# Kernel optimization log

Hardware: AMD Instinct MI355X
Metric: run time of the kernel (lower is better)

The kernel has to match this reference:

```python
import jax, jax.numpy as jnp
import numpy as np

BETA = 1.0
DECAY = 0.95


def setup_inputs() -> dict:
    key = jax.random.key(0)
    ks = jax.random.split(key, 10)
    B, S, D = 8, 2048, 1024
    M, d = 4096, 256
    sc_in = 1.0 / np.sqrt(D)
    sc_slot = 1.0 / np.sqrt(d)
    return {
        "x": jax.random.normal(ks[0], (B, S, D), jnp.float32),
        "memory": jax.random.normal(ks[1], (B, M, d), jnp.float32) * 0.01,
        "Wq": jax.random.normal(ks[2], (D, d), jnp.float32) * sc_in,
        "bq": jnp.zeros((d,), jnp.float32),
        "Wv": jax.random.normal(ks[3], (D, d), jnp.float32) * sc_in,
        "bv": jnp.zeros((d,), jnp.float32),
        "Wo": jax.random.normal(ks[4], (d, D), jnp.float32) * sc_slot,
        "bo": jnp.zeros((D,), jnp.float32),
        "Wg": jax.random.normal(ks[5], (D, 1), jnp.float32) * sc_in,
        "bg": jnp.zeros((1,), jnp.float32),
    }


def reference(x, memory, Wq, bq, Wv, bv, Wo, bo, Wg, bg):
    # ---- shared summary + query ----
    x_summary = jnp.mean(x, axis=1)                      # [B, D]
    query = x_summary @ Wq + bq                          # [B, d]

    # ---- read: Hopfield retrieval against memory[0] (shared patterns) ----
    patterns = memory[0]                                 # [M, d]
    read_scores = BETA * (query @ patterns.T)            # [B, M]
    read_attn = jax.nn.softmax(read_scores, axis=-1)
    retrieved = read_attn @ patterns                     # [B, d]
    read_out = retrieved @ Wo + bo                       # [B, D]
    x_augmented = x + read_out[:, None, :]               # broadcast over seq

    # ---- write: gated EMA update to per-batch memory ----
    write_value = x_summary @ Wv + bv                    # [B, d]
    write_gate = jax.nn.sigmoid(x_summary @ Wg + bg)     # [B, 1]
    w_scores = BETA * jnp.einsum('bd,bmd->bm', query, memory)
    w_attn = jax.nn.softmax(w_scores, axis=-1)           # [B, M]
    update = write_gate[:, :, None] * write_value[:, None, :]   # [B, 1, d]
    weighted_update = w_attn[:, :, None] * update        # [B, M, d]
    memory_new = DECAY * memory + (1.0 - DECAY) * weighted_update

    return x_augmented, memory_new
```

## Files before the change

### kernel.cpp

```cpp
#include <hip/hip_runtime.h>
#include <math.h>

#define BB 8
#define SS 2048
#define DD 1024
#define MM 4096
#define dd 256
#define NCH 64
#define CS (SS/NCH)

#define OFF_PART  0
#define OFF_Q     524288
#define OFF_WV    526336
#define OFF_GATE  528384
#define OFF_COMBO 528392
#define OFF_SUMS  528400
#define OFF_SC    528416
#define OFF_PRET  593952
#define OFF_ROUT  725024

__global__ void k1(const float* __restrict__ x, float* __restrict__ ws) {
    int blk = blockIdx.x;
    int chunk = blk & 63;
    int b = blk >> 6;
    int t = threadIdx.x;
    const float4* x4 = (const float4*)(x + ((size_t)b*SS + (size_t)chunk*CS)*DD);
    float4 a = make_float4(0.f,0.f,0.f,0.f);
    #pragma unroll 8
    for (int s = 0; s < CS; ++s) {
        float4 v = x4[s*(DD/4) + t];
        a.x += v.x; a.y += v.y; a.z += v.z; a.w += v.w;
    }
    ((float4*)(ws + OFF_PART))[(size_t)(b*NCH + chunk)*256 + t] = a;
}

__global__ void k23(const float* __restrict__ Wq, const float* __restrict__ bq,
                    const float* __restrict__ Wv, const float* __restrict__ bv,
                    const float* __restrict__ Wg, const float* __restrict__ bg,
                    float* __restrict__ ws) {
    __shared__ float4 xsA[256];
    __shared__ float4 xsB[256];
    __shared__ float red[512];
    int blk = blockIdx.x;
    int t = threadIdx.x;
    if (blk < 64) {
        int cs = blk & 3;
        int wb = blk >> 2;
        int b = wb & 7;
        int which = wb >> 3;
        int col4 = t & 255;
        int half = t >> 8;
        const float4* p4 = (const float4*)(ws + OFF_PART);
        float4 a = make_float4(0.f,0.f,0.f,0.f);
        #pragma unroll 8
        for (int c = 0; c < 32; ++c) {
            float4 v = p4[(size_t)(b*NCH + half*32 + c)*256 + col4];
            a.x += v.x; a.y += v.y; a.z += v.z; a.w += v.w;
        }
        if (half == 0) xsA[col4] = a; else xsB[col4] = a;
        __syncthreads();
        if (t < 256) {
            float4 u = xsA[t], v = xsB[t];
            xsA[t] = make_float4((u.x+v.x)*(1.f/SS), (u.y+v.y)*(1.f/SS),
                                 (u.z+v.z)*(1.f/SS), (u.w+v.w)*(1.f/SS));
        }
        __syncthreads();
        const float* xs = (const float*)xsA;
        const float* W = which ? Wv : Wq;
        int kg = t >> 6;
        int c0 = cs*64 + (t & 63);
        float acc = 0.f;
        #pragma unroll 8
        for (int kk = 0; kk < 128; ++kk) {
            int k = kg*128 + kk;
            acc += xs[k] * W[(size_t)k*dd + c0];
        }
        red[t] = acc;
        __syncthreads();
        if (t < 64) {
            int c = cs*64 + t;
            float o = red[t] + red[t+64] + red[t+128] + red[t+192]
                    + red[t+256] + red[t+320] + red[t+384] + red[t+448];
            o += which ? bv[c] : bq[c];
            ws[(which ? OFF_WV : OFF_Q) + b*dd + c] = o;
        }
    } else {
        int b = blk - 64;
        const float* base = ws + OFF_PART + (size_t)(b*NCH)*DD;
        float wg0 = Wg[t], wg1 = Wg[t + 512];
        float acc = 0.f;
        #pragma unroll 8
        for (int c = 0; c < NCH; ++c) {
            const float* p = base + (size_t)c*DD;
            acc += p[t]*wg0 + p[t+512]*wg1;
        }
        red[t] = acc; __syncthreads();
        for (int s2 = 256; s2 > 0; s2 >>= 1) {
            if (t < s2) red[t] += red[t + s2];
            __syncthreads();
        }
        if (t == 0)
            ws[OFF_GATE + b] = 1.f / (1.f + __expf(-(red[0]*(1.f/SS) + bg[0])));
    }
}

__global__ void k4(const float* __restrict__ memory, float* __restrict__ ws) {
    int wave = threadIdx.x >> 6;
    int lane = threadIdx.x & 63;
    int task = blockIdx.x*4 + wave;
    int m = task & (MM-1);
    int b = (task >> 12) & 7;
    int which = task >> 15;
    const float* row = (which == 0) ? (memory + (size_t)m*dd)
                                    : (memory + ((size_t)b*MM + m)*dd);
    const float4 a  = ((const float4*)row)[lane];
    const float4 qv = ((const float4*)(ws + OFF_Q + b*dd))[lane];
    float p = a.x*qv.x + a.y*qv.y + a.z*qv.z + a.w*qv.w;
    #pragma unroll
    for (int off = 32; off > 0; off >>= 1) p += __shfl_xor(p, off);
    if (lane == 0) ws[OFF_SC + (size_t)(which*BB + b)*MM + m] = __expf(p);
}

__global__ void k5(const float* __restrict__ memory, float* __restrict__ ws) {
    __shared__ float red[256];
    int blk = blockIdx.x;
    int t = threadIdx.x;
    if (blk < 16) {
        const float4* p = (const float4*)(ws + OFF_SC + (size_t)blk*MM);
        float s = 0.f;
        #pragma unroll
        for (int i = 0; i < 4; ++i) {
            float4 v = p[i*256 + t];
            s += v.x + v.y + v.z + v.w;
        }
        red[t] = s; __syncthreads();
        for (int s2 = 128; s2 > 0; s2 >>= 1) {
            if (t < s2) red[t] += red[t + s2];
            __syncthreads();
        }
        if (t == 0) ws[OFF_SUMS + blk] = red[0];
    } else {
        int idx = blk - 16;
        int mc = idx & 63;
        int b = idx >> 6;
        if (t < 64) red[t] = ws[OFF_SC + (size_t)b*MM + mc*64 + t];
        __syncthreads();
        float acc = 0.f;
        const float* pat = memory + (size_t)mc*64*dd + t;
        #pragma unroll 8
        for (int i = 0; i < 64; ++i) acc += red[i] * pat[(size_t)i*dd];
        ws[OFF_PRET + (size_t)(b*64 + mc)*dd + t] = acc;
    }
}

__global__ void k7(const float* __restrict__ Wo, const float* __restrict__ bo,
                   float* __restrict__ ws) {
    __shared__ float ret[dd];
    __shared__ float red[256];
    int blk = blockIdx.x;
    int cb = blk & 15;
    int b = blk >> 4;
    int t = threadIdx.x;
    float acc0 = 0.f;
    #pragma unroll 8
    for (int mc = 0; mc < 64; ++mc)
        acc0 += ws[OFF_PRET + (size_t)(b*64 + mc)*dd + t];
    ret[t] = acc0 / ws[OFF_SUMS + b];
    if (cb == 0 && t == 0)
        ws[OFF_COMBO + b] = 0.05f * ws[OFF_GATE + b] / ws[OFF_SUMS + BB + b];
    __syncthreads();
    int c = t & 63, jr = t >> 6;
    float acc = 0.f;
    #pragma unroll 8
    for (int jj = 0; jj < 64; ++jj) {
        int j = jr*64 + jj;
        acc += ret[j] * Wo[(size_t)j*DD + cb*64 + c];
    }
    red[t] = acc; __syncthreads();
    if (t < 64) {
        ws[OFF_ROUT + (size_t)b*DD + cb*64 + t] =
            red[t] + red[t+64] + red[t+128] + red[t+192] + bo[cb*64 + t];
    }
}

__global__ void k8(const float* __restrict__ x, const float* __restrict__ memory,
                   const float* __restrict__ ws, float* __restrict__ out) {
    const int NA = BB*SS*DD/4;
    const int NT = NA + BB*MM*dd/4;
    const float4* x4 = (const float4*)x;
    const float4* m4 = (const float4*)memory;
    const float4* r4 = (const float4*)(ws + OFF_ROUT);
    const float4* w4 = (const float4*)(ws + OFF_WV);
    float4* o4 = (float4*)out;
    int stride = gridDim.x * blockDim.x;
    for (int i = blockIdx.x*blockDim.x + threadIdx.x; i < NT; i += stride) {
        if (i < NA) {
            int b = i >> 19;
            int c = i & 255;
            float4 xv = x4[i];
            float4 rv = r4[(b << 8) + c];
            o4[i] = make_float4(xv.x+rv.x, xv.y+rv.y, xv.z+rv.z, xv.w+rv.w);
        } else {
            int j = i - NA;
            int b = j >> 18;
            int m = (j >> 6) & (MM-1);
            int d4 = j & 63;
            float coeff = ws[OFF_COMBO + b] * ws[OFF_SC + (size_t)(BB + b)*MM + m];
            float4 wv = w4[(b << 6) + d4];
            float4 mv = m4[j];
            o4[i] = make_float4(0.95f*mv.x + coeff*wv.x,
                                0.95f*mv.y + coeff*wv.y,
                                0.95f*mv.z + coeff*wv.z,
                                0.95f*mv.w + coeff*wv.w);
        }
    }
}

extern "C" void kernel_launch(void* const* d_in, const int* in_sizes, int n_in,
                              void* d_out, int out_size, void* d_ws, size_t ws_size,
                              hipStream_t stream) {
    const float* x      = (const float*)d_in[0];
    const float* memory = (const float*)d_in[1];
    const float* Wq     = (const float*)d_in[2];
    const float* bq     = (const float*)d_in[3];
    const float* Wv     = (const float*)d_in[4];
    const float* bv     = (const float*)d_in[5];
    const float* Wo     = (const float*)d_in[6];
    const float* bo     = (const float*)d_in[7];
    const float* Wg     = (const float*)d_in[8];
    const float* bg     = (const float*)d_in[9];
    float* out = (float*)d_out;
    float* ws  = (float*)d_ws;

    k1<<<BB*NCH, 256, 0, stream>>>(x, ws);
    k23<<<72, 512, 0, stream>>>(Wq, bq, Wv, bv, Wg, bg, ws);
    k4<<<2*BB*MM/4, 256, 0, stream>>>(memory, ws);
    k5<<<16 + BB*64, 256, 0, stream>>>(memory, ws);
    k7<<<BB*16, 256, 0, stream>>>(Wo, bo, ws);
    k8<<<4096, 256, 0, stream>>>(x, memory, ws, out);
}
```

Before: 76.76 us.

## Fuse score, partial-sum and retrieval kernels into one tiled kernel

Merges the per-row score kernel and the sum/retrieval kernel into a single kernel. Each block handles a 64-row memory tile: it computes exp scores into shared memory, writes a per-tile partial sum, and either does the pattern-weighted retrieval (read path) or stores the scores (write path). The final sums are then reduced inside k7, so one launch goes away and the exp scores no longer make a round trip through global memory for the retrieval step. The cost is a longer per-block serial loop over 64 rows and a little extra reduction work in k7.

```diff
diff --git a/kernel.cpp b/kernel.cpp
--- a/kernel.cpp
+++ b/kernel.cpp
@@ -14,10 +14,10 @@
 #define OFF_WV    526336
 #define OFF_GATE  528384
 #define OFF_COMBO 528392
-#define OFF_SUMS  528400
-#define OFF_SC    528416
-#define OFF_PRET  593952
-#define OFF_ROUT  725024
+#define OFF_SUMP  528400
+#define OFF_SC    529424
+#define OFF_PRET  562192
+#define OFF_ROUT  693264
 
 __global__ void k1(const float* __restrict__ x, float* __restrict__ ws) {
     int blk = blockIdx.x;
@@ -43,6 +43,7 @@
     __shared__ float red[512];
     int blk = blockIdx.x;
     int t = threadIdx.x;
+    const float4* p4 = (const float4*)(ws + OFF_PART);
     if (blk < 64) {
         int cs = blk & 3;
         int wb = blk >> 2;
@@ -50,7 +51,6 @@
         int which = wb >> 3;
         int col4 = t & 255;
         int half = t >> 8;
-        const float4* p4 = (const float4*)(ws + OFF_PART);
         float4 a = make_float4(0.f,0.f,0.f,0.f);
         #pragma unroll 8
         for (int c = 0; c < 32; ++c) {
@@ -104,52 +104,40 @@
     }
 }
 
-__global__ void k4(const float* __restrict__ memory, float* __restrict__ ws) {
-    int wave = threadIdx.x >> 6;
-    int lane = threadIdx.x & 63;
-    int task = blockIdx.x*4 + wave;
-    int m = task & (MM-1);
-    int b = (task >> 12) & 7;
-    int which = task >> 15;
-    const float* row = (which == 0) ? (memory + (size_t)m*dd)
-                                    : (memory + ((size_t)b*MM + m)*dd);
-    const float4 a  = ((const float4*)row)[lane];
+__global__ void k45(const float* __restrict__ memory, float* __restrict__ ws) {
+    __shared__ float esc[64];
+    int idx = blockIdx.x;
+    int which = idx >> 9;
+    int b = (idx >> 6) & 7;
+    int mc = idx & 63;
+    int t = threadIdx.x;
+    int wave = t >> 6, lane = t & 63;
+    const float* tile = ((which == 0) ? memory : memory + (size_t)b*MM*dd)
+                        + (size_t)mc*64*dd;
     const float4 qv = ((const float4*)(ws + OFF_Q + b*dd))[lane];
-    float p = a.x*qv.x + a.y*qv.y + a.z*qv.z + a.w*qv.w;
-    #pragma unroll
-    for (int off = 32; off > 0; off >>= 1) p += __shfl_xor(p, off);
-    if (lane == 0) ws[OFF_SC + (size_t)(which*BB + b)*MM + m] = __expf(p);
-}
-
-__global__ void k5(const float* __restrict__ memory, float* __restrict__ ws) {
-    __shared__ float red[256];
-    int blk = blockIdx.x;
-    int t = threadIdx.x;
-    if (blk < 16) {
-        const float4* p = (const float4*)(ws + OFF_SC + (size_t)blk*MM);
-        float s = 0.f;
-        #pragma unroll
-        for (int i = 0; i < 4; ++i) {
-            float4 v = p[i*256 + t];
-            s += v.x + v.y + v.z + v.w;
-        }
-        red[t] = s; __syncthreads();
-        for (int s2 = 128; s2 > 0; s2 >>= 1) {
-            if (t < s2) red[t] += red[t + s2];
-            __syncthreads();
-        }
-        if (t == 0) ws[OFF_SUMS + blk] = red[0];
+    #pragma unroll 4
+    for (int i = 0; i < 16; ++i) {
+        int r = i*4 + wave;
+        float4 a = ((const float4*)(tile + (size_t)r*dd))[lane];
+        float p = a.x*qv.x + a.y*qv.y + a.z*qv.z + a.w*qv.w;
+        #pragma unroll
+        for (int off = 32; off > 0; off >>= 1) p += __shfl_xor(p, off);
+        if (lane == 0) esc[r] = __expf(p);
+    }
+    __syncthreads();
+    if (t < 64) {
+        float v = esc[t];
+        #pragma unroll
+        for (int off = 32; off > 0; off >>= 1) v += __shfl_xor(v, off);
+        if (t == 0) ws[OFF_SUMP + which*512 + b*64 + mc] = v;
+    }
+    if (which == 0) {
+        float acc = 0.f;
+        #pragma unroll 8
+        for (int i = 0; i < 64; ++i) acc += esc[i] * tile[(size_t)i*dd + t];
+        ws[OFF_PRET + (size_t)(b*64 + mc)*dd + t] = acc;
     } else {
-        int idx = blk - 16;
-        int mc = idx & 63;
-        int b = idx >> 6;
-        if (t < 64) red[t] = ws[OFF_SC + (size_t)b*MM + mc*64 + t];
-        __syncthreads();
-        float acc = 0.f;
-        const float* pat = memory + (size_t)mc*64*dd + t;
-        #pragma unroll 8
-        for (int i = 0; i < 64; ++i) acc += red[i] * pat[(size_t)i*dd];
-        ws[OFF_PRET + (size_t)(b*64 + mc)*dd + t] = acc;
+        if (t < 64) ws[OFF_SC + (size_t)b*MM + mc*64 + t] = esc[t];
     }
 }
 
@@ -157,17 +145,28 @@
                    float* __restrict__ ws) {
     __shared__ float ret[dd];
     __shared__ float red[256];
+    __shared__ float ssum;
     int blk = blockIdx.x;
     int cb = blk & 15;
     int b = blk >> 4;
     int t = threadIdx.x;
+    if (t < 64) {
+        float v = ws[OFF_SUMP + b*64 + t];
+        #pragma unroll
+        for (int off = 32; off > 0; off >>= 1) v += __shfl_xor(v, off);
+        if (t == 0) ssum = v;
+    } else if (t < 128 && cb == 0) {
+        float v = ws[OFF_SUMP + 512 + b*64 + (t - 64)];
+        #pragma unroll
+        for (int off = 32; off > 0; off >>= 1) v += __shfl_xor(v, off);
+        if (t == 64) ws[OFF_COMBO + b] = 0.05f * ws[OFF_GATE + b] / v;
+    }
     float acc0 = 0.f;
     #pragma unroll 8
     for (int mc = 0; mc < 64; ++mc)
         acc0 += ws[OFF_PRET + (size_t)(b*64 + mc)*dd + t];
-    ret[t] = acc0 / ws[OFF_SUMS + b];
-    if (cb == 0 && t == 0)
-        ws[OFF_COMBO + b] = 0.05f * ws[OFF_GATE + b] / ws[OFF_SUMS + BB + b];
+    __syncthreads();
+    ret[t] = acc0 / ssum;
     __syncthreads();
     int c = t & 63, jr = t >> 6;
     float acc = 0.f;
@@ -205,7 +204,7 @@
             int b = j >> 18;
             int m = (j >> 6) & (MM-1);
             int d4 = j & 63;
-            float coeff = ws[OFF_COMBO + b] * ws[OFF_SC + (size_t)(BB + b)*MM + m];
+            float coeff = ws[OFF_COMBO + b] * ws[OFF_SC + (size_t)b*MM + m];
             float4 wv = w4[(b << 6) + d4];
             float4 mv = m4[j];
             o4[i] = make_float4(0.95f*mv.x + coeff*wv.x,
@@ -234,8 +233,7 @@
 
     k1<<<BB*NCH, 256, 0, stream>>>(x, ws);
     k23<<<72, 512, 0, stream>>>(Wq, bq, Wv, bv, Wg, bg, ws);
-    k4<<<2*BB*MM/4, 256, 0, stream>>>(memory, ws);
-    k5<<<16 + BB*64, 256, 0, stream>>>(memory, ws);
+    k45<<<1024, 256, 0, stream>>>(memory, ws);
     k7<<<BB*16, 256, 0, stream>>>(Wo, bo, ws);
     k8<<<4096, 256, 0, stream>>>(x, memory, ws, out);
 }
```

Measured after the change: 73.80 us. -3.9%, faster.
